# Kernel optimization log

Measured on AMD Instinct MI355X. Metric: run time of the kernel, lower is better.

The kernel has to match this reference:

```python
import jax, jax.numpy as jnp
import numpy as np

B, S, D_MODEL, D_FF = 8, 1024, 512, 2048
NCAT, NSUB, TOPK = 8, 8, 2
E = NCAT * NSUB            # 64 experts
CAP = 1024


def setup_inputs() -> dict:
    key = jax.random.key(0)
    ks = jax.random.split(key, 6)
    hidden = jax.random.normal(ks[0], (B, S, D_MODEL), jnp.float32)
    cat_indices = jax.random.randint(ks[1], (B, S, TOPK), 0, NCAT)
    sub_indices = jax.random.randint(ks[2], (B, S, TOPK), 0, NSUB)
    weights = jax.random.uniform(ks[3], (B, S, TOPK), jnp.float32)
    # Stacked per-expert MLP params (Expert = Linear -> GELU -> Linear, dropout off in eval)
    W1 = jax.random.normal(ks[4], (E, D_MODEL, D_FF), jnp.float32) / np.sqrt(D_MODEL).astype(np.float32)
    b1 = jnp.zeros((E, D_FF), jnp.float32)
    W2 = jax.random.normal(ks[5], (E, D_FF, D_MODEL), jnp.float32) / np.sqrt(D_FF).astype(np.float32)
    b2 = jnp.zeros((E, D_MODEL), jnp.float32)
    return dict(hidden=hidden, cat_indices=cat_indices, sub_indices=sub_indices,
                weights=weights, W1=W1, b1=b1, W2=W2, b2=b2)


def _moe_forward(hidden, cat_indices, sub_indices, weights, W1, b1, W2, b2):
    Bq, Sq, d = hidden.shape
    K = cat_indices.shape[-1]
    T = Bq * Sq            # tokens
    A = T * K              # (token, k) routing assignments
    x = hidden.reshape(T, d)
    eid = (cat_indices * NSUB + sub_indices).reshape(A).astype(jnp.int32)  # flat expert id
    wf = weights.reshape(A)
    tok = jnp.arange(A, dtype=jnp.int32) // K  # token index per assignment

    # position of each assignment within its expert's capacity buffer
    oh = jax.nn.one_hot(eid, E, dtype=jnp.int32)                     # [A, E]
    pos = jnp.take_along_axis(jnp.cumsum(oh, axis=0) - 1,
                              eid[:, None].astype(jnp.int32), axis=1)[:, 0]
    valid = (pos < CAP).astype(hidden.dtype)

    # dispatch: gather tokens into [E, CAP, d] buffer (overflow dropped; CAP sized to avoid it)
    buf = jnp.zeros((E, CAP, d), hidden.dtype).at[eid, pos].set(x[tok], mode='drop')

    # grouped expert MLP: Linear -> GELU -> Linear
    h = jax.nn.gelu(jnp.einsum('ecd,edf->ecf', buf, W1) + b1[:, None, :], approximate=False)
    yb = jnp.einsum('ecf,efd->ecd', h, W2) + b2[:, None, :]          # [E, CAP, d]

    # combine: gather each assignment's expert output, weight it, scatter-add over tokens
    pc = jnp.minimum(pos, CAP - 1)
    ya = yb[eid, pc] * (wf * valid)[:, None]                          # [A, d]
    out = jnp.zeros((T, d), hidden.dtype).at[tok].add(ya)
    return out.reshape(Bq, Sq, d)


def reference(hidden, cat_indices, sub_indices, weights, W1, b1, W2, b2):
    return _moe_forward(hidden, cat_indices, sub_indices, weights, W1, b1, W2, b2)
```

## Files before the change

### kernel.cpp

```cpp
#include <hip/hip_runtime.h>
#include <hip/hip_bf16.h>
#include <cstdint>
#include <cstddef>

#define TOKENS 8192
#define ASSIGN 16384
#define DM     512
#define DFF    2048
#define NEXP   64
#define NSUB_  8
#define CAP2   512

#define BM 256
#define BN 128
#define BK 64

typedef __bf16 bf16;
typedef __bf16 bf16x4 __attribute__((ext_vector_type(4)));
typedef __bf16 bf16x8 __attribute__((ext_vector_type(8)));
typedef float  f32x4  __attribute__((ext_vector_type(4)));

__global__ void k_zero(int* __restrict__ count) { count[threadIdx.x] = 0; }

__global__ void k_route(const int* __restrict__ cat, const int* __restrict__ sub,
                        int* __restrict__ count, int* __restrict__ slot_of) {
    int a = blockIdx.x * 256 + threadIdx.x;
    if (a >= ASSIGN) return;
    int e = cat[a] * NSUB_ + sub[a];
    int s = atomicAdd(&count[e], 1);
    slot_of[a] = (s < CAP2) ? (e * CAP2 + s) : -1;
}

__global__ void k_gather(const float* __restrict__ hidden, const int* __restrict__ slot_of,
                         bf16* __restrict__ xg) {
    int a = blockIdx.x;
    int r = slot_of[a];
    if (r < 0) return;
    int tok = a >> 1;
    int t = threadIdx.x;
    const f32x4* src = (const f32x4*)(hidden + (size_t)tok * DM);
    f32x4 v0 = src[t * 2], v1 = src[t * 2 + 1];
    bf16x8 o;
    o[0] = (bf16)v0[0]; o[1] = (bf16)v0[1]; o[2] = (bf16)v0[2]; o[3] = (bf16)v0[3];
    o[4] = (bf16)v1[0]; o[5] = (bf16)v1[1]; o[6] = (bf16)v1[2]; o[7] = (bf16)v1[3];
    *(bf16x8*)(xg + (size_t)r * DM + t * 8) = o;
}

__device__ inline void gload_lds16(const void* g, void* l) {
    __builtin_amdgcn_global_load_lds((const __attribute__((address_space(1))) void*)g,
                                     (__attribute__((address_space(3))) void*)l, 16, 0, 0);
}

template <bool GELU>
__global__ __launch_bounds__(512) void k_gemm(const bf16* __restrict__ A,
                                              const float* __restrict__ W,
                                              const float* __restrict__ bias,
                                              bf16* __restrict__ C,
                                              const int* __restrict__ count, int N, int K) {
    __shared__ __align__(16) char As0[BM * BK * 2];
    __shared__ __align__(16) char As1[BM * BK * 2];
    __shared__ __align__(16) char Bs[BN * BK * 2];

    int e = blockIdx.z, mtile = blockIdx.y, ntile = blockIdx.x;
    int mc = count[e]; if (mc > CAP2) mc = CAP2;
    if (mtile * BM >= mc) return;
    int tid = threadIdx.x, wave = tid >> 6, lane = tid & 63;
    int wm = wave >> 1, wn = wave & 1;

    const char*  Ag = (const char*)(A + (size_t)(e * CAP2 + mtile * BM) * K);
    const float* Wg = W + (size_t)e * K * N + (size_t)ntile * BN;

    int kq = ((lane >> 3) & 7) | ((wave & 1) << 3);
    int nq = (lane & 7) | (((wave >> 1) & 3) << 3);

    f32x4 br[4];

    auto issueB = [&](int kt) {
        const float* p = Wg + (size_t)(kt * BK + kq * 4) * N + nq * 4;
        br[0] = *(const f32x4*)(p);
        br[1] = *(const f32x4*)(p + N);
        br[2] = *(const f32x4*)(p + 2 * (size_t)N);
        br[3] = *(const f32x4*)(p + 3 * (size_t)N);
    };
    auto issueA = [&](int kt, char* dst) {
#pragma unroll
        for (int i = 0; i < 4; i++) {
            int chunk = i * 8 + wave;
            int d = chunk * 1024 + lane * 16;
            int row = d >> 7;
            int col = (d & 127) ^ ((row & 7) << 4);
            gload_lds16(Ag + (size_t)row * (2 * K) + (size_t)kt * 128 + col,
                        dst + chunk * 1024);
        }
    };
    auto writeB = [&]() {
#pragma unroll
        for (int c = 0; c < 4; c++) {
            int n = nq * 4 + c;
            bf16x4 v;
#pragma unroll
            for (int j = 0; j < 4; j++) v[j] = (bf16)br[j][c];
            *(bf16x4*)(Bs + n * 128 + ((kq * 8) ^ ((n & 7) << 4))) = v;
        }
    };

    f32x4 acc[4][4];
#pragma unroll
    for (int i = 0; i < 4; i++)
#pragma unroll
        for (int j = 0; j < 4; j++) acc[i][j] = f32x4{0.f, 0.f, 0.f, 0.f};

    auto mfmaTile = [&](const char* Ab) {
#pragma unroll
        for (int ks = 0; ks < 2; ks++) {
            bf16x8 af[4], bfv[4];
#pragma unroll
            for (int mi = 0; mi < 4; mi++) {
                int row = wm * 64 + mi * 16 + (lane & 15);
                af[mi] = *(const bf16x8*)(Ab + row * 128 +
                         ((ks * 64 + (lane >> 4) * 16) ^ ((row & 7) << 4)));
            }
#pragma unroll
            for (int ni = 0; ni < 4; ni++) {
                int row = wn * 64 + ni * 16 + (lane & 15);
                bfv[ni] = *(const bf16x8*)(Bs + row * 128 +
                          ((ks * 64 + (lane >> 4) * 16) ^ ((row & 7) << 4)));
            }
#pragma unroll
            for (int mi = 0; mi < 4; mi++)
#pragma unroll
                for (int ni = 0; ni < 4; ni++)
                    acc[mi][ni] = __builtin_amdgcn_mfma_f32_16x16x32_bf16(
                        af[mi], bfv[ni], acc[mi][ni], 0, 0, 0);
        }
    };

    issueA(0, As0);
    issueB(0);
    asm volatile("s_waitcnt vmcnt(0)" ::: "memory");
    __syncthreads();
    writeB();
    __syncthreads();

    char* Acur = As0; char* Anx = As1;
    int nK = K >> 6;
    for (int kt = 0; kt < nK; kt++) {
        int nxt = (kt + 1 < nK) ? kt + 1 : kt;
        issueA(nxt, Anx);
        issueB(nxt);
        mfmaTile(Acur);
        asm volatile("s_waitcnt vmcnt(0)" ::: "memory");
        __syncthreads();
        writeB();
        __syncthreads();
        char* t = Acur; Acur = Anx; Anx = t;
    }

#pragma unroll
    for (int mi = 0; mi < 4; mi++) {
        int rowb = wm * 64 + mi * 16 + ((lane >> 4) << 2);
#pragma unroll
        for (int ni = 0; ni < 4; ni++) {
            int col = ntile * BN + wn * 64 + ni * 16 + (lane & 15);
            float bv = bias[e * N + col];
#pragma unroll
            for (int r = 0; r < 4; r++) {
                float v = acc[mi][ni][r] + bv;
                if (GELU) v = 0.5f * v * (1.0f + erff(v * 0.70710678118654752f));
                int grow = e * CAP2 + mtile * BM + rowb + r;
                C[(size_t)grow * N + col] = (bf16)v;
            }
        }
    }
}

__global__ void k_combine(const float* __restrict__ wts, const int* __restrict__ slot_of,
                          const bf16* __restrict__ y, float* __restrict__ out) {
    int tok = blockIdx.x, t = threadIdx.x;
    float acc[8] = {0, 0, 0, 0, 0, 0, 0, 0};
#pragma unroll
    for (int k = 0; k < 2; k++) {
        int a = tok * 2 + k;
        int r = slot_of[a];
        if (r >= 0) {
            float w = wts[a];
            bf16x8 v = *(const bf16x8*)(y + (size_t)r * DM + t * 8);
#pragma unroll
            for (int j = 0; j < 8; j++) acc[j] += w * (float)v[j];
        }
    }
    f32x4* o = (f32x4*)(out + (size_t)tok * DM + t * 8);
    o[0] = f32x4{acc[0], acc[1], acc[2], acc[3]};
    o[1] = f32x4{acc[4], acc[5], acc[6], acc[7]};
}

extern "C" void kernel_launch(void* const* d_in, const int* in_sizes, int n_in,
                              void* d_out, int out_size, void* d_ws, size_t ws_size,
                              hipStream_t stream) {
    const float* hidden = (const float*)d_in[0];
    const int*   cat    = (const int*)d_in[1];
    const int*   sub    = (const int*)d_in[2];
    const float* wts    = (const float*)d_in[3];
    const float* W1     = (const float*)d_in[4];
    const float* b1     = (const float*)d_in[5];
    const float* W2     = (const float*)d_in[6];
    const float* b2     = (const float*)d_in[7];
    float* out = (float*)d_out;

    char* ws = (char*)d_ws;
    size_t off = 0;
    bf16* hbuf = (bf16*)(ws + off); off += (size_t)NEXP * CAP2 * DFF * 2;
    bf16* xg   = (bf16*)(ws + off); off += (size_t)NEXP * CAP2 * DM * 2;
    bf16* y    = xg;
    int* count   = (int*)(ws + off); off += 256;
    int* slot_of = (int*)(ws + off); off += (size_t)ASSIGN * 4;

    k_zero<<<1, 64, 0, stream>>>(count);
    k_route<<<ASSIGN / 256, 256, 0, stream>>>(cat, sub, count, slot_of);
    k_gather<<<ASSIGN, 64, 0, stream>>>(hidden, slot_of, xg);

    dim3 gg1(DFF / BN, CAP2 / BM, NEXP);
    k_gemm<true><<<gg1, 512, 0, stream>>>(xg, W1, b1, hbuf, count, DFF, DM);

    dim3 gg2(DM / BN, CAP2 / BM, NEXP);
    k_gemm<false><<<gg2, 512, 0, stream>>>(hbuf, W2, b2, y, count, DM, DFF);

    k_combine<<<TOKENS, 64, 0, stream>>>(wts, slot_of, y, out);
}
```

Measured before the change: 347.2 us.

## Template GEMM on wave count, single-buffer A, and shrink GEMM2 tile

Makes the expert GEMM templated on wave count and min waves per EU. GEMM2 now runs 256-thread blocks with 128-row M tiles, giving more blocks for the small-N second GEMM, and each thread loads more B fragments. The double-buffered A tile becomes a single buffer loaded inside each k-step, with explicit barriers and sched_barriers. This cuts LDS and register use to raise occupancy, but gives up overlap of A loads with MFMA work inside a block.

```diff
diff --git a/kernel.cpp b/kernel.cpp
--- a/kernel.cpp
+++ b/kernel.cpp
@@ -10,10 +10,7 @@
 #define NEXP   64
 #define NSUB_  8
 #define CAP2   512
-
-#define BM 256
-#define BN 128
-#define BK 64
+#define BK     64
 
 typedef __bf16 bf16;
 typedef __bf16 bf16x4 __attribute__((ext_vector_type(4)));
@@ -51,58 +48,64 @@
                                      (__attribute__((address_space(3))) void*)l, 16, 0, 0);
 }
 
-template <bool GELU>
-__global__ __launch_bounds__(512) void k_gemm(const bf16* __restrict__ A,
-                                              const float* __restrict__ W,
-                                              const float* __restrict__ bias,
-                                              bf16* __restrict__ C,
-                                              const int* __restrict__ count, int N, int K) {
-    __shared__ __align__(16) char As0[BM * BK * 2];
-    __shared__ __align__(16) char As1[BM * BK * 2];
-    __shared__ __align__(16) char Bs[BN * BK * 2];
+template <int WAVES, int MINW, bool GELU>
+__global__ __launch_bounds__(WAVES * 64, MINW)
+void k_gemm(const bf16* __restrict__ A, const float* __restrict__ W,
+            const float* __restrict__ bias, bf16* __restrict__ C,
+            const int* __restrict__ count, int N, int K) {
+    constexpr int TBM = WAVES * 32;
+    constexpr int S   = 512 / (WAVES * 64);
+    __shared__ __align__(16) char As[TBM * 128];
+    __shared__ __align__(16) char Bs[128 * 128];
 
     int e = blockIdx.z, mtile = blockIdx.y, ntile = blockIdx.x;
     int mc = count[e]; if (mc > CAP2) mc = CAP2;
-    if (mtile * BM >= mc) return;
+    if (mtile * TBM >= mc) return;
     int tid = threadIdx.x, wave = tid >> 6, lane = tid & 63;
     int wm = wave >> 1, wn = wave & 1;
 
-    const char*  Ag = (const char*)(A + (size_t)(e * CAP2 + mtile * BM) * K);
-    const float* Wg = W + (size_t)e * K * N + (size_t)ntile * BN;
+    const char*  Ag = (const char*)(A + (size_t)(e * CAP2 + mtile * TBM) * K);
+    const float* Wg = W + (size_t)e * K * N + (size_t)ntile * 128;
 
     int kq = ((lane >> 3) & 7) | ((wave & 1) << 3);
-    int nq = (lane & 7) | (((wave >> 1) & 3) << 3);
-
-    f32x4 br[4];
-
+
+    f32x4 br[S][4];
     auto issueB = [&](int kt) {
-        const float* p = Wg + (size_t)(kt * BK + kq * 4) * N + nq * 4;
-        br[0] = *(const f32x4*)(p);
-        br[1] = *(const f32x4*)(p + N);
-        br[2] = *(const f32x4*)(p + 2 * (size_t)N);
-        br[3] = *(const f32x4*)(p + 3 * (size_t)N);
+#pragma unroll
+        for (int s = 0; s < S; s++) {
+            int nq = (lane & 7) + 8 * ((wave >> 1) + (WAVES / 2) * s);
+            const float* p = Wg + (size_t)(kt * BK + kq * 4) * N + nq * 4;
+            br[s][0] = *(const f32x4*)(p);
+            br[s][1] = *(const f32x4*)(p + N);
+            br[s][2] = *(const f32x4*)(p + 2 * (size_t)N);
+            br[s][3] = *(const f32x4*)(p + 3 * (size_t)N);
+        }
     };
-    auto issueA = [&](int kt, char* dst) {
+    auto writeB = [&]() {
+#pragma unroll
+        for (int s = 0; s < S; s++) {
+            int nq = (lane & 7) + 8 * ((wave >> 1) + (WAVES / 2) * s);
+#pragma unroll
+            for (int c = 0; c < 4; c++) {
+                int n = nq * 4 + c;
+                bf16x4 v;
+#pragma unroll
+                for (int j = 0; j < 4; j++) v[j] = (bf16)br[s][j][c];
+                *(bf16x4*)(Bs + n * 128 + ((kq * 8) ^ ((n & 7) << 4))) = v;
+            }
+        }
+    };
+    auto issueA = [&](int kt) {
 #pragma unroll
         for (int i = 0; i < 4; i++) {
-            int chunk = i * 8 + wave;
+            int chunk = i * WAVES + wave;
             int d = chunk * 1024 + lane * 16;
             int row = d >> 7;
             int col = (d & 127) ^ ((row & 7) << 4);
             gload_lds16(Ag + (size_t)row * (2 * K) + (size_t)kt * 128 + col,
-                        dst + chunk * 1024);
+                        As + chunk * 1024);
         }
     };
-    auto writeB = [&]() {
-#pragma unroll
-        for (int c = 0; c < 4; c++) {
-            int n = nq * 4 + c;
-            bf16x4 v;
-#pragma unroll
-            for (int j = 0; j < 4; j++) v[j] = (bf16)br[j][c];
-            *(bf16x4*)(Bs + n * 128 + ((kq * 8) ^ ((n & 7) << 4))) = v;
-        }
-    };
 
     f32x4 acc[4][4];
 #pragma unroll
@@ -110,14 +113,23 @@
 #pragma unroll
         for (int j = 0; j < 4; j++) acc[i][j] = f32x4{0.f, 0.f, 0.f, 0.f};
 
-    auto mfmaTile = [&](const char* Ab) {
+    issueB(0);
+    int nK = K >> 6;
+    for (int kt = 0; kt < nK; kt++) {
+        issueA(kt);
+        asm volatile("s_waitcnt vmcnt(0)" ::: "memory");
+        writeB();
+        if (kt + 1 < nK) issueB(kt + 1);
+        asm volatile("s_waitcnt lgkmcnt(0)" ::: "memory");
+        __builtin_amdgcn_s_barrier();
+        __builtin_amdgcn_sched_barrier(0);
 #pragma unroll
         for (int ks = 0; ks < 2; ks++) {
             bf16x8 af[4], bfv[4];
 #pragma unroll
             for (int mi = 0; mi < 4; mi++) {
                 int row = wm * 64 + mi * 16 + (lane & 15);
-                af[mi] = *(const bf16x8*)(Ab + row * 128 +
+                af[mi] = *(const bf16x8*)(As + row * 128 +
                          ((ks * 64 + (lane >> 4) * 16) ^ ((row & 7) << 4)));
             }
 #pragma unroll
@@ -133,27 +145,8 @@
                     acc[mi][ni] = __builtin_amdgcn_mfma_f32_16x16x32_bf16(
                         af[mi], bfv[ni], acc[mi][ni], 0, 0, 0);
         }
-    };
-
-    issueA(0, As0);
-    issueB(0);
-    asm volatile("s_waitcnt vmcnt(0)" ::: "memory");
-    __syncthreads();
-    writeB();
-    __syncthreads();
-
-    char* Acur = As0; char* Anx = As1;
-    int nK = K >> 6;
-    for (int kt = 0; kt < nK; kt++) {
-        int nxt = (kt + 1 < nK) ? kt + 1 : kt;
-        issueA(nxt, Anx);
-        issueB(nxt);
-        mfmaTile(Acur);
-        asm volatile("s_waitcnt vmcnt(0)" ::: "memory");
-        __syncthreads();
-        writeB();
-        __syncthreads();
-        char* t = Acur; Acur = Anx; Anx = t;
+        __builtin_amdgcn_sched_barrier(0);
+        __builtin_amdgcn_s_barrier();
     }
 
 #pragma unroll
@@ -161,13 +154,13 @@
         int rowb = wm * 64 + mi * 16 + ((lane >> 4) << 2);
 #pragma unroll
         for (int ni = 0; ni < 4; ni++) {
-            int col = ntile * BN + wn * 64 + ni * 16 + (lane & 15);
+            int col = ntile * 128 + wn * 64 + ni * 16 + (lane & 15);
             float bv = bias[e * N + col];
 #pragma unroll
             for (int r = 0; r < 4; r++) {
                 float v = acc[mi][ni][r] + bv;
                 if (GELU) v = 0.5f * v * (1.0f + erff(v * 0.70710678118654752f));
-                int grow = e * CAP2 + mtile * BM + rowb + r;
+                int grow = e * CAP2 + mtile * TBM + rowb + r;
                 C[(size_t)grow * N + col] = (bf16)v;
             }
         }
@@ -219,11 +212,11 @@
     k_route<<<ASSIGN / 256, 256, 0, stream>>>(cat, sub, count, slot_of);
     k_gather<<<ASSIGN, 64, 0, stream>>>(hidden, slot_of, xg);
 
-    dim3 gg1(DFF / BN, CAP2 / BM, NEXP);
-    k_gemm<true><<<gg1, 512, 0, stream>>>(xg, W1, b1, hbuf, count, DFF, DM);
-
-    dim3 gg2(DM / BN, CAP2 / BM, NEXP);
-    k_gemm<false><<<gg2, 512, 0, stream>>>(hbuf, W2, b2, y, count, DM, DFF);
+    dim3 gg1(DFF / 128, CAP2 / 256, NEXP);
+    k_gemm<8, 4, true><<<gg1, 512, 0, stream>>>(xg, W1, b1, hbuf, count, DFF, DM);
+
+    dim3 gg2(DM / 128, CAP2 / 128, NEXP);
+    k_gemm<4, 3, false><<<gg2, 256, 0, stream>>>(hbuf, W2, b2, y, count, DM, DFF);
 
     k_combine<<<TOKENS, 64, 0, stream>>>(wts, slot_of, y, out);
 }
```

After: 389.2 us. +12.1%, slower.
